# Optimization experiments

Hardware: AMD Instinct MI355X
Metric: run time of the kernel (lower is better)

The kernel has to match this reference:

```python
import jax, jax.numpy as jnp
import numpy as np

SCALE = 10.0
KB = 1.0  # kernel_bandwidth

B, D, P, M, K = 128, 128, 4, 100000, 10


def _sqdist(a, b):
    # a: [..., N, D], b: [..., M, D] -> squared euclidean [..., N, M]
    a2 = jnp.sum(a * a, axis=-1)[..., :, None]
    b2 = jnp.sum(b * b, axis=-1)[..., None, :]
    ab = jnp.einsum('...nd,...md->...nm', a, b)
    return jnp.maximum(a2 + b2 - 2.0 * ab, 0.0)


def setup_inputs() -> dict:
    key = jax.random.key(0)
    k1, k2, k3, k4, k5, k6, k7 = jax.random.split(key, 7)
    return {
        'global_img_feat': jax.random.normal(k1, (B, D), jnp.float32),
        'global_text_feat': jax.random.normal(k2, (B, D), jnp.float32),
        'local_img_feats': jax.random.normal(k3, (P, B, D), jnp.float32),
        'centers': jax.random.normal(k4, (P, M, D), jnp.float32),
        'cross_indices': jax.random.randint(k5, (B, K), 0, M, jnp.int64),
        'position': jax.random.randint(k6, (B,), 0, M, jnp.int64),
        'memory_vid': jax.random.randint(k7, (M,), 0, 1000, jnp.int64),
    }


def reference(global_img_feat, global_text_feat, local_img_feats, centers,
              cross_indices, position, memory_vid):
    b = global_img_feat.shape[0]
    # ---- global MMD alignment (text branch detached) ----
    img = global_img_feat / jnp.linalg.norm(global_img_feat, axis=1, keepdims=True)
    txt_d = jax.lax.stop_gradient(global_text_feat)
    txt = txt_d / jnp.linalg.norm(txt_d, axis=1, keepdims=True)
    inv2kb2 = 1.0 / (2.0 * KB * KB)
    k_xx = jnp.exp(-_sqdist(img, img) * inv2kb2)
    k_yy = jnp.exp(-_sqdist(txt, txt) * inv2kb2)
    k_xy = jnp.exp(-_sqdist(img, txt) * inv2kb2)
    off = ~jnp.eye(b, dtype=bool)
    denom = b * (b - 1)
    mmd = (jnp.sum(jnp.where(off, k_xx, 0.0)) / denom
           + jnp.sum(jnp.where(off, k_yy, 0.0)) / denom
           - 2.0 * jnp.mean(k_xy))
    # ---- local part contrastive loss (vectorized over P parts) ----
    m = centers.shape[1]
    pos_feat = centers[:, cross_indices]                       # [P,B,K,D]
    f2 = jnp.sum(local_img_feats ** 2, axis=-1)                # [P,B]
    p2 = jnp.sum(pos_feat ** 2, axis=-1)                       # [P,B,K]
    fp = jnp.einsum('pbd,pbkd->pbk', local_img_feats, pos_feat)
    pos_dist = jnp.sqrt(jnp.maximum(f2[..., None] + p2 - 2.0 * fp, 0.0))  # [P,B,K]
    neg_dist = jnp.sqrt(_sqdist(local_img_feats, centers))     # [P,B,M]
    # negative mask over memory slots (int indices are constants)
    neg_mask = jnp.ones((m,), bool).at[cross_indices.reshape(-1)].set(False)
    neg_mask = neg_mask.at[position].set(False)
    x = jnp.log(jnp.sum(jnp.exp(-SCALE * pos_dist), axis=-1))  # [P,B]
    y = jnp.log(jnp.sum(jnp.exp(-SCALE * neg_dist) * neg_mask[None, None, :], axis=-1))
    l = jnp.sum(-x + y, axis=1) / local_img_feats.shape[1]     # [P]
    l = jnp.where(jnp.isnan(l), 0.0, l)
    local_loss = jnp.sum(l) / local_img_feats.shape[0]
    total = local_loss + 1.0 * mmd
    pos_vid = memory_vid[cross_indices]                        # [B,K]
    return total, local_loss, mmd, pos_vid
```

## Files before the change

### kernel.cpp

```cpp
#include <hip/hip_runtime.h>
#include <math.h>

#define B_ 128
#define D_ 128
#define P_ 4
#define M_ 100000
#define K_ 10
#define SCALE_ 10.0f

typedef short bf16x8 __attribute__((ext_vector_type(8)));
typedef float floatx4 __attribute__((ext_vector_type(4)));

__device__ inline unsigned pack_bf16_trunc(unsigned f0, unsigned f1) {
    return __builtin_amdgcn_perm(f1, f0, 0x07060302u);
}

__device__ inline float waveReduceSum(float v) {
    #pragma unroll
    for (int off = 32; off > 0; off >>= 1) v += __shfl_xor(v, off, 64);
    return v;
}

__device__ inline float blockReduce128(float v, float* sh2) {
    v = waveReduceSum(v);
    int wid = threadIdx.x >> 6;
    if ((threadIdx.x & 63) == 0) sh2[wid] = v;
    __syncthreads();
    float r = sh2[0] + sh2[1];
    __syncthreads();
    return r;
}

__global__ __launch_bounds__(128) void k_norm(const float* __restrict__ img,
                                              const float* __restrict__ txt,
                                              float* img_n, float* txt_n,
                                              float* a2i, float* a2t,
                                              float* s_neg) {
    __shared__ float sh2[2];
    int row = blockIdx.x & 127, which = blockIdx.x >> 7;
    int t = threadIdx.x;
    if (blockIdx.x < 4) s_neg[blockIdx.x * 128 + t] = 0.f;
    const float* src = which ? txt : img;
    float* dst = which ? txt_n : img_n;
    float* a2  = which ? a2t : a2i;
    float v = src[row * D_ + t];
    float s = blockReduce128(v * v, sh2);
    float n = v / sqrtf(s);
    dst[row * D_ + t] = n;
    float s2 = blockReduce128(n * n, sh2);
    if (t == 0) a2[row] = s2;
}

__global__ __launch_bounds__(128) void k_mmd(const float* __restrict__ img_n,
                                             const float* __restrict__ txt_n,
                                             const float* __restrict__ a2i,
                                             const float* __restrict__ a2t,
                                             double* __restrict__ mmd_part) {
    __shared__ float ri[D_], rt[D_];
    __shared__ float sh2[2];
    int i = blockIdx.x, j = threadIdx.x;
    ri[j] = img_n[i * D_ + j];
    rt[j] = txt_n[i * D_ + j];
    __syncthreads();
    const float* aj = img_n + j * D_;
    const float* bj = txt_n + j * D_;
    float dxx = 0.f, dyy = 0.f, dxy = 0.f;
    #pragma unroll 4
    for (int d = 0; d < D_; d++) {
        float av = aj[d], bv = bj[d];
        dxx = fmaf(ri[d], av, dxx);
        dyy = fmaf(rt[d], bv, dyy);
        dxy = fmaf(ri[d], bv, dxy);
    }
    float kxx = (i == j) ? 0.f : expf(-fmaxf(a2i[i] + a2i[j] - 2.f * dxx, 0.f) * 0.5f);
    float kyy = (i == j) ? 0.f : expf(-fmaxf(a2t[i] + a2t[j] - 2.f * dyy, 0.f) * 0.5f);
    float kxy = expf(-fmaxf(a2i[i] + a2t[j] - 2.f * dxy, 0.f) * 0.5f);
    float sxx = blockReduce128(kxx, sh2);
    float syy = blockReduce128(kyy, sh2);
    float sxy = blockReduce128(kxy, sh2);
    if (j == 0) {
        mmd_part[i] = (double)sxx;
        mmd_part[128 + i] = (double)syy;
        mmd_part[256 + i] = (double)sxy;
    }
}

__global__ __launch_bounds__(64) void k_pos(const float* __restrict__ local,
                                            const float* __restrict__ centers,
                                            const int* __restrict__ ci,
                                            const int* __restrict__ memory_vid,
                                            float* f2w, float* s_pos, float* out) {
    int p = blockIdx.x >> 7, b = blockIdx.x & 127;
    int t = threadIdx.x;
    const float* f = local + ((size_t)p * B_ + b) * D_;
    float f0 = f[t], f1 = f[t + 64];
    float f2v = waveReduceSum(f0 * f0 + f1 * f1);
    if (t == 0) f2w[p * B_ + b] = f2v;
    float s = 0.f;
    for (int k = 0; k < K_; k++) {
        int idx = ci[b * K_ + k];
        const float* c = centers + ((size_t)p * M_ + idx) * D_;
        float c0 = c[t], c1 = c[t + 64];
        float p2 = waveReduceSum(c0 * c0 + c1 * c1);
        float fp = waveReduceSum(f0 * c0 + f1 * c1);
        float d2 = fmaxf(f2v + p2 - 2.f * fp, 0.f);
        s += expf(-SCALE_ * sqrtf(d2));
    }
    if (t == 0) s_pos[p * B_ + b] = s;
    if (p == 0 && t < K_) {
        int idx = ci[b * K_ + t];
        out[3 + b * K_ + t] = (float)memory_vid[idx];
    }
}

#define TM_ 128
__global__ __launch_bounds__(256, 3) void k_neg(const float* __restrict__ local,
                                                const float* __restrict__ centers,
                                                const float* __restrict__ f2w,
                                                const int* __restrict__ ci,
                                                const int* __restrict__ pos,
                                                float* __restrict__ s_neg) {
    const int p = blockIdx.y;
    const int m0 = blockIdx.x * TM_;
    const int t = threadIdx.x;
    const int w = t >> 6;
    const int l = t & 63;
    const int n16 = l & 15;
    const int q = l >> 4;

    __shared__ bf16x8 A_lds[2048];
    __shared__ float sred[512];
    __shared__ unsigned char msk[TM_];

    const float* lp = local + (size_t)p * B_ * D_;
    #pragma unroll
    for (int s8 = 0; s8 < 8; s8++) {
        int f = t + 256 * s8;
        int fl = f & 63, bt = (f >> 6) & 7, kc = f >> 9;
        int row = bt * 16 + (fl & 15);
        int col = kc * 32 + ((fl >> 4) & 3) * 8;
        const uint4 u0 = *(const uint4*)(lp + row * D_ + col);
        const uint4 u1 = *(const uint4*)(lp + row * D_ + col + 4);
        union { bf16x8 v; unsigned u[4]; } fr;
        fr.u[0] = pack_bf16_trunc(u0.x, u0.y);
        fr.u[1] = pack_bf16_trunc(u0.z, u0.w);
        fr.u[2] = pack_bf16_trunc(u1.x, u1.y);
        fr.u[3] = pack_bf16_trunc(u1.z, u1.w);
        A_lds[f] = fr.v;
    }
    if (t < TM_) msk[t] = 1;
    __syncthreads();

    int gm[2];
    gm[0] = m0 + (w * 2 + 0) * 16 + n16;
    gm[1] = m0 + (w * 2 + 1) * 16 + n16;
    const float* cb = centers + (size_t)p * M_ * D_;
    uint4 rb[2][4][2];
    if (m0 + TM_ <= M_) {
        #pragma unroll
        for (int wm = 0; wm < 2; wm++) {
            const uint4* src = (const uint4*)(cb + (size_t)gm[wm] * D_ + q * 8);
            #pragma unroll
            for (int kc = 0; kc < 4; kc++) {
                rb[wm][kc][0] = src[kc * 8];
                rb[wm][kc][1] = src[kc * 8 + 1];
            }
        }
    } else {
        const uint4 z = make_uint4(0u, 0u, 0u, 0u);
        #pragma unroll
        for (int wm = 0; wm < 2; wm++) {
            const uint4* src = (const uint4*)(cb + (size_t)gm[wm] * D_ + q * 8);
            #pragma unroll
            for (int kc = 0; kc < 4; kc++) {
                if (gm[wm] < M_) {
                    rb[wm][kc][0] = src[kc * 8];
                    rb[wm][kc][1] = src[kc * 8 + 1];
                } else {
                    rb[wm][kc][0] = z;
                    rb[wm][kc][1] = z;
                }
            }
        }
    }

    #pragma unroll
    for (int i = 0; i < 5; i++) {
        int idx = ci[t + 256 * i];
        unsigned r = (unsigned)(idx - m0);
        if (r < TM_) msk[r] = 0;
    }
    if (t < B_) {
        unsigned r = (unsigned)(pos[t] - m0);
        if (r < TM_) msk[r] = 0;
    }

    float c2a[2];
    bf16x8 bfr[2][4];
    #pragma unroll
    for (int wm = 0; wm < 2; wm++) {
        float c = 0.f;
        #pragma unroll
        for (int kc = 0; kc < 4; kc++) {
            union { uint4 u; floatx4 f; } a, b;
            a.u = rb[wm][kc][0];
            b.u = rb[wm][kc][1];
            c += a.f[0]*a.f[0] + a.f[1]*a.f[1] + a.f[2]*a.f[2] + a.f[3]*a.f[3]
               + b.f[0]*b.f[0] + b.f[1]*b.f[1] + b.f[2]*b.f[2] + b.f[3]*b.f[3];
            union { bf16x8 v; unsigned u[4]; } fr;
            fr.u[0] = pack_bf16_trunc(a.u.x, a.u.y);
            fr.u[1] = pack_bf16_trunc(a.u.z, a.u.w);
            fr.u[2] = pack_bf16_trunc(b.u.x, b.u.y);
            fr.u[3] = pack_bf16_trunc(b.u.z, b.u.w);
            bfr[wm][kc] = fr.v;
        }
        c2a[wm] = c;
    }

    floatx4 acc[8][2];
    #pragma unroll
    for (int bt = 0; bt < 8; bt++) {
        acc[bt][0] = (floatx4)(0.f);
        acc[bt][1] = (floatx4)(0.f);
    }
    #pragma unroll
    for (int kc = 0; kc < 4; kc++) {
        #pragma unroll
        for (int bt = 0; bt < 8; bt++) {
            bf16x8 af = A_lds[kc * 512 + bt * 64 + l];
            acc[bt][0] = __builtin_amdgcn_mfma_f32_16x16x32_bf16(af, bfr[0][kc], acc[bt][0], 0, 0, 0);
            acc[bt][1] = __builtin_amdgcn_mfma_f32_16x16x32_bf16(af, bfr[1][kc], acc[bt][1], 0, 0, 0);
        }
    }

    float c2v[2], vmul[2];
    #pragma unroll
    for (int wm = 0; wm < 2; wm++) {
        float c = c2a[wm];
        c += __shfl_xor(c, 16, 64);
        c += __shfl_xor(c, 32, 64);
        c2v[wm] = c;
        vmul[wm] = (gm[wm] < M_ && msk[(w * 2 + wm) * 16 + n16] != 0) ? 1.f : 0.f;
    }

    const float* f2p = f2w + p * B_;
    #pragma unroll
    for (int bt = 0; bt < 8; bt++) {
        #pragma unroll
        for (int r = 0; r < 4; r++) {
            int b = bt * 16 + q * 4 + r;
            float f2v = f2p[b];
            float s = 0.f;
            #pragma unroll
            for (int wm = 0; wm < 2; wm++) {
                float d2 = fmaxf(f2v + c2v[wm] - 2.f * acc[bt][wm][r], 0.f);
                s += vmul[wm] * expf(-SCALE_ * sqrtf(d2));
            }
            s += __shfl_xor(s, 1, 64);
            s += __shfl_xor(s, 2, 64);
            s += __shfl_xor(s, 4, 64);
            s += __shfl_xor(s, 8, 64);
            if (n16 == 0) sred[w * 128 + b] = s;
        }
    }
    __syncthreads();
    if (t < 128) {
        float s = sred[t] + sred[128 + t] + sred[256 + t] + sred[384 + t];
        atomicAdd(&s_neg[p * B_ + t], s);
    }
}

__global__ __launch_bounds__(512) void k_final(const float* __restrict__ s_pos,
                                               const float* __restrict__ s_neg,
                                               const double* __restrict__ mmd_part,
                                               float* out) {
    __shared__ float red[512];
    __shared__ float lp_[4];
    int t = threadIdx.x;
    float x = logf(s_pos[t]);
    float y = logf(s_neg[t]);
    red[t] = -x + y;
    __syncthreads();
    for (int s = 64; s > 0; s >>= 1) {
        if ((t & 127) < s) red[t] += red[t + s];
        __syncthreads();
    }
    if ((t & 127) == 0) {
        float l = red[t] / (float)B_;
        if (isnan(l)) l = 0.f;
        lp_[t >> 7] = l;
    }
    __syncthreads();
    if (t == 0) {
        float local_loss = (lp_[0] + lp_[1] + lp_[2] + lp_[3]) / (float)P_;
        double sxx = 0.0, syy = 0.0, sxy = 0.0;
        for (int i = 0; i < 128; i++) {
            sxx += mmd_part[i];
            syy += mmd_part[128 + i];
            sxy += mmd_part[256 + i];
        }
        double denom = 128.0 * 127.0;
        float mmd = (float)(sxx / denom + syy / denom - 2.0 * (sxy / (128.0 * 128.0)));
        out[0] = local_loss + mmd;
        out[1] = local_loss;
        out[2] = mmd;
    }
}

extern "C" void kernel_launch(void* const* d_in, const int* in_sizes, int n_in,
                              void* d_out, int out_size, void* d_ws, size_t ws_size,
                              hipStream_t stream) {
    const float* img     = (const float*)d_in[0];
    const float* txt     = (const float*)d_in[1];
    const float* local   = (const float*)d_in[2];
    const float* centers = (const float*)d_in[3];
    const int*   ci      = (const int*)d_in[4];
    const int*   pos     = (const int*)d_in[5];
    const int*   mvid    = (const int*)d_in[6];
    float* out = (float*)d_out;

    char* ws = (char*)d_ws;
    float*  img_n    = (float*)(ws + 0);
    float*  txt_n    = (float*)(ws + 65536);
    float*  a2i      = (float*)(ws + 131072);
    float*  a2t      = (float*)(ws + 131584);
    float*  f2w      = (float*)(ws + 132096);
    float*  s_pos    = (float*)(ws + 134144);
    float*  s_neg    = (float*)(ws + 136192);
    double* mmd_part = (double*)(ws + 138240);

    k_norm<<<256, 128, 0, stream>>>(img, txt, img_n, txt_n, a2i, a2t, s_neg);
    k_mmd<<<128, 128, 0, stream>>>(img_n, txt_n, a2i, a2t, mmd_part);
    k_pos<<<P_ * B_, 64, 0, stream>>>(local, centers, ci, mvid, f2w, s_pos, out);
    dim3 gneg((M_ + TM_ - 1) / TM_, P_);
    k_neg<<<gneg, 256, 0, stream>>>(local, centers, f2w, ci, pos, s_neg);
    k_final<<<1, 512, 0, stream>>>(s_pos, s_neg, mmd_part, out);
}
```

Baseline: 379.5 us.

## Fuse MMD, positive and negative kernels; skip negligible exp terms by distance cutoff

```diff
diff --git a/kernel.cpp b/kernel.cpp
--- a/kernel.cpp
+++ b/kernel.cpp
@@ -7,6 +7,11 @@
 #define M_ 100000
 #define K_ 10
 #define SCALE_ 10.0f
+#define MB_ 782
+#define NEG_BLOCKS (MB_ * P_)
+#define MMD_BLOCKS 128
+#define POS_BLOCKS 128
+#define D2_CUT 120.0f
 
 typedef short bf16x8 __attribute__((ext_vector_type(8)));
 typedef float floatx4 __attribute__((ext_vector_type(4)));
@@ -15,14 +20,31 @@
     return __builtin_amdgcn_perm(f1, f0, 0x07060302u);
 }
 
-__device__ inline float waveReduceSum(float v) {
+template <int CTRL>
+__device__ inline float dpp_add(float v) {
+    int x = __builtin_amdgcn_update_dpp(0, __builtin_bit_cast(int, v), CTRL, 0xF, 0xF, true);
+    return v + __builtin_bit_cast(float, x);
+}
+__device__ inline float row16Sum(float v) {
+    v = dpp_add<0xB1>(v);
+    v = dpp_add<0x4E>(v);
+    v = dpp_add<0x141>(v);
+    v = dpp_add<0x140>(v);
+    return v;
+}
+__device__ inline float waveSum64(float v) {
+    v = row16Sum(v);
+    v += __shfl_xor(v, 16, 64);
+    v += __shfl_xor(v, 32, 64);
+    return v;
+}
+__device__ inline float waveReduceSumOld(float v) {
     #pragma unroll
     for (int off = 32; off > 0; off >>= 1) v += __shfl_xor(v, off, 64);
     return v;
 }
-
 __device__ inline float blockReduce128(float v, float* sh2) {
-    v = waveReduceSum(v);
+    v = waveSum64(v);
     int wid = threadIdx.x >> 6;
     if ((threadIdx.x & 63) == 0) sh2[wid] = v;
     __syncthreads();
@@ -31,242 +53,287 @@
     return r;
 }
 
-__global__ __launch_bounds__(128) void k_norm(const float* __restrict__ img,
+__global__ __launch_bounds__(128) void k_prep(const float* __restrict__ img,
                                               const float* __restrict__ txt,
-                                              float* img_n, float* txt_n,
+                                              const float* __restrict__ local,
+                                              float* imgT, float* txtT,
                                               float* a2i, float* a2t,
-                                              float* s_neg) {
+                                              float* f2w, float* s_neg) {
     __shared__ float sh2[2];
-    int row = blockIdx.x & 127, which = blockIdx.x >> 7;
-    int t = threadIdx.x;
-    if (blockIdx.x < 4) s_neg[blockIdx.x * 128 + t] = 0.f;
-    const float* src = which ? txt : img;
-    float* dst = which ? txt_n : img_n;
-    float* a2  = which ? a2t : a2i;
-    float v = src[row * D_ + t];
-    float s = blockReduce128(v * v, sh2);
-    float n = v / sqrtf(s);
-    dst[row * D_ + t] = n;
-    float s2 = blockReduce128(n * n, sh2);
-    if (t == 0) a2[row] = s2;
-}
-
-__global__ __launch_bounds__(128) void k_mmd(const float* __restrict__ img_n,
-                                             const float* __restrict__ txt_n,
-                                             const float* __restrict__ a2i,
-                                             const float* __restrict__ a2t,
-                                             double* __restrict__ mmd_part) {
-    __shared__ float ri[D_], rt[D_];
-    __shared__ float sh2[2];
-    int i = blockIdx.x, j = threadIdx.x;
-    ri[j] = img_n[i * D_ + j];
-    rt[j] = txt_n[i * D_ + j];
-    __syncthreads();
-    const float* aj = img_n + j * D_;
-    const float* bj = txt_n + j * D_;
-    float dxx = 0.f, dyy = 0.f, dxy = 0.f;
-    #pragma unroll 4
-    for (int d = 0; d < D_; d++) {
-        float av = aj[d], bv = bj[d];
-        dxx = fmaf(ri[d], av, dxx);
-        dyy = fmaf(rt[d], bv, dyy);
-        dxy = fmaf(ri[d], bv, dxy);
+    int bid = blockIdx.x, t = threadIdx.x;
+    if (bid < 256) {
+        int row = bid & 127, which = bid >> 7;
+        if (bid < 4) s_neg[bid * 128 + t] = 0.f;
+        const float* src = which ? txt : img;
+        float* dstT = which ? txtT : imgT;
+        float* a2 = which ? a2t : a2i;
+        float v = src[row * D_ + t];
+        float s = blockReduce128(v * v, sh2);
+        float n = v / sqrtf(s);
+        dstT[t * 128 + row] = n;
+        float s2 = blockReduce128(n * n, sh2);
+        if (t == 0) a2[row] = s2;
+    } else {
+        int r = bid - 256;
+        float v = local[(size_t)r * D_ + t];
+        float s = blockReduce128(v * v, sh2);
+        if (t == 0) f2w[r] = s;
     }
-    float kxx = (i == j) ? 0.f : expf(-fmaxf(a2i[i] + a2i[j] - 2.f * dxx, 0.f) * 0.5f);
-    float kyy = (i == j) ? 0.f : expf(-fmaxf(a2t[i] + a2t[j] - 2.f * dyy, 0.f) * 0.5f);
-    float kxy = expf(-fmaxf(a2i[i] + a2t[j] - 2.f * dxy, 0.f) * 0.5f);
-    float sxx = blockReduce128(kxx, sh2);
-    float syy = blockReduce128(kyy, sh2);
-    float sxy = blockReduce128(kxy, sh2);
-    if (j == 0) {
-        mmd_part[i] = (double)sxx;
-        mmd_part[128 + i] = (double)syy;
-        mmd_part[256 + i] = (double)sxy;
-    }
-}
-
-__global__ __launch_bounds__(64) void k_pos(const float* __restrict__ local,
-                                            const float* __restrict__ centers,
-                                            const int* __restrict__ ci,
-                                            const int* __restrict__ memory_vid,
-                                            float* f2w, float* s_pos, float* out) {
-    int p = blockIdx.x >> 7, b = blockIdx.x & 127;
-    int t = threadIdx.x;
-    const float* f = local + ((size_t)p * B_ + b) * D_;
-    float f0 = f[t], f1 = f[t + 64];
-    float f2v = waveReduceSum(f0 * f0 + f1 * f1);
-    if (t == 0) f2w[p * B_ + b] = f2v;
-    float s = 0.f;
-    for (int k = 0; k < K_; k++) {
-        int idx = ci[b * K_ + k];
-        const float* c = centers + ((size_t)p * M_ + idx) * D_;
-        float c0 = c[t], c1 = c[t + 64];
-        float p2 = waveReduceSum(c0 * c0 + c1 * c1);
-        float fp = waveReduceSum(f0 * c0 + f1 * c1);
-        float d2 = fmaxf(f2v + p2 - 2.f * fp, 0.f);
-        s += expf(-SCALE_ * sqrtf(d2));
-    }
-    if (t == 0) s_pos[p * B_ + b] = s;
-    if (p == 0 && t < K_) {
-        int idx = ci[b * K_ + t];
-        out[3 + b * K_ + t] = (float)memory_vid[idx];
-    }
-}
-
-#define TM_ 128
-__global__ __launch_bounds__(256, 3) void k_neg(const float* __restrict__ local,
-                                                const float* __restrict__ centers,
-                                                const float* __restrict__ f2w,
-                                                const int* __restrict__ ci,
-                                                const int* __restrict__ pos,
-                                                float* __restrict__ s_neg) {
-    const int p = blockIdx.y;
-    const int m0 = blockIdx.x * TM_;
+}
+
+__global__ __launch_bounds__(256, 4) void k_main(const float* __restrict__ local,
+                                                 const float* __restrict__ centers,
+                                                 const float* __restrict__ imgT,
+                                                 const float* __restrict__ txtT,
+                                                 const float* __restrict__ a2i,
+                                                 const float* __restrict__ a2t,
+                                                 const int* __restrict__ ci,
+                                                 const int* __restrict__ posi,
+                                                 const int* __restrict__ mvid,
+                                                 const float* __restrict__ f2w,
+                                                 float* __restrict__ s_neg,
+                                                 float* __restrict__ s_pos,
+                                                 double* __restrict__ mmd_part,
+                                                 float* __restrict__ out) {
+    union Smem {
+        struct {
+            bf16x8 A_lds[2048];
+            float sred[512];
+            float f2l[128];
+            unsigned char msk[128];
+        } n;
+        struct {
+            float ri[128], rt[128];
+            float sh2[2];
+        } m;
+    };
+    __shared__ Smem sm;
+    const int bid = blockIdx.x;
     const int t = threadIdx.x;
     const int w = t >> 6;
     const int l = t & 63;
-    const int n16 = l & 15;
-    const int q = l >> 4;
-
-    __shared__ bf16x8 A_lds[2048];
-    __shared__ float sred[512];
-    __shared__ unsigned char msk[TM_];
-
-    const float* lp = local + (size_t)p * B_ * D_;
-    #pragma unroll
-    for (int s8 = 0; s8 < 8; s8++) {
-        int f = t + 256 * s8;
-        int fl = f & 63, bt = (f >> 6) & 7, kc = f >> 9;
-        int row = bt * 16 + (fl & 15);
-        int col = kc * 32 + ((fl >> 4) & 3) * 8;
-        const uint4 u0 = *(const uint4*)(lp + row * D_ + col);
-        const uint4 u1 = *(const uint4*)(lp + row * D_ + col + 4);
-        union { bf16x8 v; unsigned u[4]; } fr;
-        fr.u[0] = pack_bf16_trunc(u0.x, u0.y);
-        fr.u[1] = pack_bf16_trunc(u0.z, u0.w);
-        fr.u[2] = pack_bf16_trunc(u1.x, u1.y);
-        fr.u[3] = pack_bf16_trunc(u1.z, u1.w);
-        A_lds[f] = fr.v;
-    }
-    if (t < TM_) msk[t] = 1;
-    __syncthreads();
-
-    int gm[2];
-    gm[0] = m0 + (w * 2 + 0) * 16 + n16;
-    gm[1] = m0 + (w * 2 + 1) * 16 + n16;
-    const float* cb = centers + (size_t)p * M_ * D_;
-    uint4 rb[2][4][2];
-    if (m0 + TM_ <= M_) {
-        #pragma unroll
-        for (int wm = 0; wm < 2; wm++) {
-            const uint4* src = (const uint4*)(cb + (size_t)gm[wm] * D_ + q * 8);
-            #pragma unroll
-            for (int kc = 0; kc < 4; kc++) {
-                rb[wm][kc][0] = src[kc * 8];
-                rb[wm][kc][1] = src[kc * 8 + 1];
-            }
-        }
-    } else {
-        const uint4 z = make_uint4(0u, 0u, 0u, 0u);
-        #pragma unroll
-        for (int wm = 0; wm < 2; wm++) {
-            const uint4* src = (const uint4*)(cb + (size_t)gm[wm] * D_ + q * 8);
-            #pragma unroll
-            for (int kc = 0; kc < 4; kc++) {
-                if (gm[wm] < M_) {
+
+    if (bid < NEG_BLOCKS) {
+        const int p = bid / MB_;
+        const int mb = bid - p * MB_;
+        const int m0 = mb * 128;
+        const int n16 = l & 15;
+        const int q = l >> 4;
+
+        const float* lp = local + (size_t)p * B_ * D_;
+        if (t < 128) { sm.n.msk[t] = 1; sm.n.f2l[t] = f2w[p * 128 + t]; }
+        #pragma unroll
+        for (int s8 = 0; s8 < 8; s8++) {
+            int f = t + 256 * s8;
+            int fl = f & 63, bt = (f >> 6) & 7, kc = f >> 9;
+            int row = bt * 16 + (fl & 15);
+            int col = kc * 32 + ((fl >> 4) & 3) * 8;
+            const uint4 u0 = *(const uint4*)(lp + row * D_ + col);
+            const uint4 u1 = *(const uint4*)(lp + row * D_ + col + 4);
+            union { bf16x8 v; unsigned u[4]; } fr;
+            fr.u[0] = pack_bf16_trunc(u0.x, u0.y);
+            fr.u[1] = pack_bf16_trunc(u0.z, u0.w);
+            fr.u[2] = pack_bf16_trunc(u1.x, u1.y);
+            fr.u[3] = pack_bf16_trunc(u1.z, u1.w);
+            sm.n.A_lds[f] = fr.v;
+        }
+        __syncthreads();
+
+        int gm[2];
+        gm[0] = m0 + (w * 2 + 0) * 16 + n16;
+        gm[1] = m0 + (w * 2 + 1) * 16 + n16;
+        const float* cb = centers + (size_t)p * M_ * D_;
+        uint4 rb[2][4][2];
+        if (m0 + 128 <= M_) {
+            #pragma unroll
+            for (int wm = 0; wm < 2; wm++) {
+                const uint4* src = (const uint4*)(cb + (size_t)gm[wm] * D_ + q * 8);
+                #pragma unroll
+                for (int kc = 0; kc < 4; kc++) {
                     rb[wm][kc][0] = src[kc * 8];
                     rb[wm][kc][1] = src[kc * 8 + 1];
-                } else {
-                    rb[wm][kc][0] = z;
-                    rb[wm][kc][1] = z;
                 }
             }
-        }
-    }
-
-    #pragma unroll
-    for (int i = 0; i < 5; i++) {
-        int idx = ci[t + 256 * i];
-        unsigned r = (unsigned)(idx - m0);
-        if (r < TM_) msk[r] = 0;
-    }
-    if (t < B_) {
-        unsigned r = (unsigned)(pos[t] - m0);
-        if (r < TM_) msk[r] = 0;
-    }
-
-    float c2a[2];
-    bf16x8 bfr[2][4];
-    #pragma unroll
-    for (int wm = 0; wm < 2; wm++) {
-        float c = 0.f;
+        } else {
+            const uint4 z = make_uint4(0u, 0u, 0u, 0u);
+            #pragma unroll
+            for (int wm = 0; wm < 2; wm++) {
+                const uint4* src = (const uint4*)(cb + (size_t)gm[wm] * D_ + q * 8);
+                #pragma unroll
+                for (int kc = 0; kc < 4; kc++) {
+                    if (gm[wm] < M_) {
+                        rb[wm][kc][0] = src[kc * 8];
+                        rb[wm][kc][1] = src[kc * 8 + 1];
+                    } else {
+                        rb[wm][kc][0] = z;
+                        rb[wm][kc][1] = z;
+                    }
+                }
+            }
+        }
+
+        #pragma unroll
+        for (int i = 0; i < 5; i++) {
+            int idx = ci[t + 256 * i];
+            unsigned r = (unsigned)(idx - m0);
+            if (r < 128u) sm.n.msk[r] = 0;
+        }
+        if (t < B_) {
+            unsigned r = (unsigned)(posi[t] - m0);
+            if (r < 128u) sm.n.msk[r] = 0;
+        }
+        __syncthreads();
+
+        float c2a[2];
+        bf16x8 bfr[2][4];
+        #pragma unroll
+        for (int wm = 0; wm < 2; wm++) {
+            float c = 0.f;
+            #pragma unroll
+            for (int kc = 0; kc < 4; kc++) {
+                union { uint4 u; floatx4 f; } a, b;
+                a.u = rb[wm][kc][0];
+                b.u = rb[wm][kc][1];
+                c += a.f[0]*a.f[0] + a.f[1]*a.f[1] + a.f[2]*a.f[2] + a.f[3]*a.f[3]
+                   + b.f[0]*b.f[0] + b.f[1]*b.f[1] + b.f[2]*b.f[2] + b.f[3]*b.f[3];
+                union { bf16x8 v; unsigned u[4]; } fr;
+                fr.u[0] = pack_bf16_trunc(a.u.x, a.u.y);
+                fr.u[1] = pack_bf16_trunc(a.u.z, a.u.w);
+                fr.u[2] = pack_bf16_trunc(b.u.x, b.u.y);
+                fr.u[3] = pack_bf16_trunc(b.u.z, b.u.w);
+                bfr[wm][kc] = fr.v;
+            }
+            c2a[wm] = c;
+        }
+
+        floatx4 acc[8][2];
+        #pragma unroll
+        for (int bt = 0; bt < 8; bt++) { acc[bt][0] = (floatx4)(0.f); acc[bt][1] = (floatx4)(0.f); }
         #pragma unroll
         for (int kc = 0; kc < 4; kc++) {
-            union { uint4 u; floatx4 f; } a, b;
-            a.u = rb[wm][kc][0];
-            b.u = rb[wm][kc][1];
-            c += a.f[0]*a.f[0] + a.f[1]*a.f[1] + a.f[2]*a.f[2] + a.f[3]*a.f[3]
-               + b.f[0]*b.f[0] + b.f[1]*b.f[1] + b.f[2]*b.f[2] + b.f[3]*b.f[3];
-            union { bf16x8 v; unsigned u[4]; } fr;
-            fr.u[0] = pack_bf16_trunc(a.u.x, a.u.y);
-            fr.u[1] = pack_bf16_trunc(a.u.z, a.u.w);
-            fr.u[2] = pack_bf16_trunc(b.u.x, b.u.y);
-            fr.u[3] = pack_bf16_trunc(b.u.z, b.u.w);
-            bfr[wm][kc] = fr.v;
-        }
-        c2a[wm] = c;
-    }
-
-    floatx4 acc[8][2];
-    #pragma unroll
-    for (int bt = 0; bt < 8; bt++) {
-        acc[bt][0] = (floatx4)(0.f);
-        acc[bt][1] = (floatx4)(0.f);
-    }
-    #pragma unroll
-    for (int kc = 0; kc < 4; kc++) {
+            #pragma unroll
+            for (int bt = 0; bt < 8; bt++) {
+                bf16x8 af = sm.n.A_lds[kc * 512 + bt * 64 + l];
+                acc[bt][0] = __builtin_amdgcn_mfma_f32_16x16x32_bf16(af, bfr[0][kc], acc[bt][0], 0, 0, 0);
+                acc[bt][1] = __builtin_amdgcn_mfma_f32_16x16x32_bf16(af, bfr[1][kc], acc[bt][1], 0, 0, 0);
+            }
+        }
+
+        float c2v[2];
+        #pragma unroll
+        for (int wm = 0; wm < 2; wm++) {
+            float c = c2a[wm];
+            c += __shfl_xor(c, 16, 64);
+            c += __shfl_xor(c, 32, 64);
+            c2v[wm] = c;
+        }
+
+        float dmin = 1e30f;
         #pragma unroll
         for (int bt = 0; bt < 8; bt++) {
-            bf16x8 af = A_lds[kc * 512 + bt * 64 + l];
-            acc[bt][0] = __builtin_amdgcn_mfma_f32_16x16x32_bf16(af, bfr[0][kc], acc[bt][0], 0, 0, 0);
-            acc[bt][1] = __builtin_amdgcn_mfma_f32_16x16x32_bf16(af, bfr[1][kc], acc[bt][1], 0, 0, 0);
-        }
-    }
-
-    float c2v[2], vmul[2];
-    #pragma unroll
-    for (int wm = 0; wm < 2; wm++) {
-        float c = c2a[wm];
-        c += __shfl_xor(c, 16, 64);
-        c += __shfl_xor(c, 32, 64);
-        c2v[wm] = c;
-        vmul[wm] = (gm[wm] < M_ && msk[(w * 2 + wm) * 16 + n16] != 0) ? 1.f : 0.f;
-    }
-
-    const float* f2p = f2w + p * B_;
-    #pragma unroll
-    for (int bt = 0; bt < 8; bt++) {
-        #pragma unroll
-        for (int r = 0; r < 4; r++) {
-            int b = bt * 16 + q * 4 + r;
-            float f2v = f2p[b];
-            float s = 0.f;
-            #pragma unroll
-            for (int wm = 0; wm < 2; wm++) {
-                float d2 = fmaxf(f2v + c2v[wm] - 2.f * acc[bt][wm][r], 0.f);
-                s += vmul[wm] * expf(-SCALE_ * sqrtf(d2));
-            }
-            s += __shfl_xor(s, 1, 64);
-            s += __shfl_xor(s, 2, 64);
-            s += __shfl_xor(s, 4, 64);
-            s += __shfl_xor(s, 8, 64);
-            if (n16 == 0) sred[w * 128 + b] = s;
-        }
-    }
-    __syncthreads();
-    if (t < 128) {
-        float s = sred[t] + sred[128 + t] + sred[256 + t] + sred[384 + t];
-        atomicAdd(&s_neg[p * B_ + t], s);
+            floatx4 f4 = *(const floatx4*)&sm.n.f2l[bt * 16 + q * 4];
+            #pragma unroll
+            for (int r = 0; r < 4; r++) {
+                float d20 = fmaf(-2.f, acc[bt][0][r], f4[r] + c2v[0]);
+                float d21 = fmaf(-2.f, acc[bt][1][r], f4[r] + c2v[1]);
+                dmin = fminf(dmin, fminf(d20, d21));
+            }
+        }
+        if (!__any(dmin < D2_CUT)) {
+            sm.n.sred[w * 128 + l] = 0.f;
+            sm.n.sred[w * 128 + l + 64] = 0.f;
+        } else {
+            float vm0 = (gm[0] < M_ && sm.n.msk[(w * 2 + 0) * 16 + n16] != 0) ? 1.f : 0.f;
+            float vm1 = (gm[1] < M_ && sm.n.msk[(w * 2 + 1) * 16 + n16] != 0) ? 1.f : 0.f;
+            #pragma unroll
+            for (int bt = 0; bt < 8; bt++) {
+                floatx4 f4 = *(const floatx4*)&sm.n.f2l[bt * 16 + q * 4];
+                #pragma unroll
+                for (int r = 0; r < 4; r++) {
+                    float s = 0.f;
+                    float d20 = fmaxf(fmaf(-2.f, acc[bt][0][r], f4[r] + c2v[0]), 0.f);
+                    float d21 = fmaxf(fmaf(-2.f, acc[bt][1][r], f4[r] + c2v[1]), 0.f);
+                    if (d20 < D2_CUT) s += vm0 * expf(-SCALE_ * sqrtf(d20));
+                    if (d21 < D2_CUT) s += vm1 * expf(-SCALE_ * sqrtf(d21));
+                    s = row16Sum(s);
+                    if (n16 == 0) sm.n.sred[w * 128 + bt * 16 + q * 4 + r] = s;
+                }
+            }
+        }
+        __syncthreads();
+        if (t < 128) {
+            float s = sm.n.sred[t] + sm.n.sred[128 + t] + sm.n.sred[256 + t] + sm.n.sred[384 + t];
+            atomicAdd(&s_neg[p * 128 + t], s);
+        }
+    } else if (bid < NEG_BLOCKS + MMD_BLOCKS) {
+        const int i = bid - NEG_BLOCKS;
+        if (t < 128) {
+            sm.m.ri[t] = imgT[t * 128 + i];
+            sm.m.rt[t] = txtT[t * 128 + i];
+        }
+        __syncthreads();
+        float kxx = 0.f, kyy = 0.f, kxy = 0.f;
+        if (t < 128) {
+            float dxx = 0.f, dyy = 0.f, dxy = 0.f;
+            #pragma unroll 4
+            for (int d = 0; d < D_; d++) {
+                float rid = sm.m.ri[d], rtd = sm.m.rt[d];
+                float av = imgT[d * 128 + t];
+                float bv = txtT[d * 128 + t];
+                dxx = fmaf(rid, av, dxx);
+                dyy = fmaf(rtd, bv, dyy);
+                dxy = fmaf(rid, bv, dxy);
+            }
+            kxx = (i == t) ? 0.f : expf(-fmaxf(a2i[i] + a2i[t] - 2.f * dxx, 0.f) * 0.5f);
+            kyy = (i == t) ? 0.f : expf(-fmaxf(a2t[i] + a2t[t] - 2.f * dyy, 0.f) * 0.5f);
+            kxy = expf(-fmaxf(a2i[i] + a2t[t] - 2.f * dxy, 0.f) * 0.5f);
+        }
+        float sxx = waveReduceSumOld(kxx);
+        float syy = waveReduceSumOld(kyy);
+        float sxy = waveReduceSumOld(kxy);
+        __syncthreads();
+        if (t == 0)  { sm.m.sh2[0] = sxx; }
+        if (t == 64) { sm.m.sh2[1] = sxx; }
+        __syncthreads();
+        float txx = sm.m.sh2[0] + sm.m.sh2[1];
+        __syncthreads();
+        if (t == 0)  { sm.m.sh2[0] = syy; }
+        if (t == 64) { sm.m.sh2[1] = syy; }
+        __syncthreads();
+        float tyy = sm.m.sh2[0] + sm.m.sh2[1];
+        __syncthreads();
+        if (t == 0)  { sm.m.sh2[0] = sxy; }
+        if (t == 64) { sm.m.sh2[1] = sxy; }
+        __syncthreads();
+        float txy = sm.m.sh2[0] + sm.m.sh2[1];
+        if (t == 0) {
+            mmd_part[i] = (double)txx;
+            mmd_part[128 + i] = (double)tyy;
+            mmd_part[256 + i] = (double)txy;
+        }
+    } else {
+        const int pair = (bid - (NEG_BLOCKS + MMD_BLOCKS)) * 4 + w;
+        const int p = pair >> 7, b = pair & 127;
+        const float* f = local + (size_t)pair * D_;
+        float f0 = f[l], f1 = f[l + 64];
+        float f2v = f2w[pair];
+        const float* cb = centers + (size_t)p * M_ * D_;
+        float s = 0.f;
+        #pragma unroll
+        for (int k = 0; k < K_; k++) {
+            int idx = ci[b * K_ + k];
+            const float* c = cb + (size_t)idx * D_;
+            float c0 = c[l], c1 = c[l + 64];
+            float p2 = waveSum64(c0 * c0 + c1 * c1);
+            float fp = waveSum64(f0 * c0 + f1 * c1);
+            float d2 = fmaxf(f2v + p2 - 2.f * fp, 0.f);
+            if (d2 < D2_CUT) s += expf(-SCALE_ * sqrtf(d2));
+        }
+        if (l == 0) s_pos[pair] = s;
+        if (p == 0 && l < K_) {
+            int ix = ci[b * K_ + l];
+            out[3 + b * K_ + l] = (float)mvid[ix];
+        }
     }
 }
 
@@ -286,9 +353,9 @@
         __syncthreads();
     }
     if ((t & 127) == 0) {
-        float l = red[t] / (float)B_;
-        if (isnan(l)) l = 0.f;
-        lp_[t >> 7] = l;
+        float lv = red[t] / (float)B_;
+        if (isnan(lv)) lv = 0.f;
+        lp_[t >> 7] = lv;
     }
     __syncthreads();
     if (t == 0) {
@@ -315,13 +382,13 @@
     const float* local   = (const float*)d_in[2];
     const float* centers = (const float*)d_in[3];
     const int*   ci      = (const int*)d_in[4];
-    const int*   pos     = (const int*)d_in[5];
+    const int*   posi    = (const int*)d_in[5];
     const int*   mvid    = (const int*)d_in[6];
     float* out = (float*)d_out;
 
     char* ws = (char*)d_ws;
-    float*  img_n    = (float*)(ws + 0);
-    float*  txt_n    = (float*)(ws + 65536);
+    float*  imgT     = (float*)(ws + 0);
+    float*  txtT     = (float*)(ws + 65536);
     float*  a2i      = (float*)(ws + 131072);
     float*  a2t      = (float*)(ws + 131584);
     float*  f2w      = (float*)(ws + 132096);
@@ -329,10 +396,9 @@
     float*  s_neg    = (float*)(ws + 136192);
     double* mmd_part = (double*)(ws + 138240);
 
-    k_norm<<<256, 128, 0, stream>>>(img, txt, img_n, txt_n, a2i, a2t, s_neg);
-    k_mmd<<<128, 128, 0, stream>>>(img_n, txt_n, a2i, a2t, mmd_part);
-    k_pos<<<P_ * B_, 64, 0, stream>>>(local, centers, ci, mvid, f2w, s_pos, out);
-    dim3 gneg((M_ + TM_ - 1) / TM_, P_);
-    k_neg<<<gneg, 256, 0, stream>>>(local, centers, f2w, ci, pos, s_neg);
+    k_prep<<<768, 128, 0, stream>>>(img, txt, local, imgT, txtT, a2i, a2t, f2w, s_neg);
+    k_main<<<NEG_BLOCKS + MMD_BLOCKS + POS_BLOCKS, 256, 0, stream>>>(
+        local, centers, imgT, txtT, a2i, a2t, ci, posi, mvid, f2w,
+        s_neg, s_pos, mmd_part, out);
     k_final<<<1, 512, 0, stream>>>(s_pos, s_neg, mmd_part, out);
 }
```

Result: faster. 345.5 us (-9.0%).
